# Kernel optimization log

Measured on AMD Instinct MI355X. Metric: run time of the kernel, lower is better.

Reference implementation:

```python
import jax, jax.numpy as jnp
import numpy as np

N, E = 30000, 180000
IN, H, OUT = 3000, 512, 30


def _segment_softmax(e, dst, n):
    # numerically stable softmax over incoming edges of each destination node
    m = jax.ops.segment_max(e, dst, num_segments=n)
    m = jnp.where(jnp.isfinite(m), m, 0.0)  # nodes with no in-edges
    ex = jnp.exp(e - m[dst])
    den = jax.ops.segment_sum(ex, dst, num_segments=n)
    return ex / den[dst]


def _gat(x, src, dst, Ws, Wd, a_s, a_d, n, alpha=None):
    """edGATConv (heads=1, no self-loops, no bias).
    xs = lin_s(x); attention score from lin_s(x)[src] and lin_d(x)[dst];
    out[i] = sum_{e: dst_e=i} alpha_e * xs[src_e].
    If alpha is given (tie_alpha), reuse it instead of recomputing."""
    xs = x @ Ws.T  # [n, F_out]
    if alpha is None:
        xd = x @ Wd.T
        e = jax.nn.leaky_relu(xs[src] @ a_s + xd[dst] @ a_d, 0.2)  # [E]
        alpha = _segment_softmax(e, dst, n)
    out = jax.ops.segment_sum(alpha[:, None] * xs[src], dst, num_segments=n)
    return out, alpha


def setup_inputs() -> dict:
    key = jax.random.key(0)
    ks = jax.random.split(key, 7)
    features = jax.random.normal(ks[0], (N, IN), dtype=jnp.float32)
    edge_index = jax.random.randint(ks[1], (2, E), 0, N)
    W1s = jax.random.normal(ks[2], (H, IN), dtype=jnp.float32) * 0.02
    W1d = jax.random.normal(ks[3], (H, IN), dtype=jnp.float32) * 0.02
    a1s = jax.random.normal(ks[4], (H,), dtype=jnp.float32) * 0.1
    a1d = jax.random.normal(ks[5], (H,), dtype=jnp.float32) * 0.1
    W2s = jax.random.normal(ks[6], (OUT, H), dtype=jnp.float32) * 0.05
    return {"features": features, "edge_index": edge_index,
            "W1s": W1s, "W1d": W1d, "a1s": a1s, "a1d": a1d, "W2s": W2s}


def reference(features, edge_index, W1s, W1d, a1s, a1d, W2s):
    src, dst = edge_index[0], edge_index[1]
    n = features.shape[0]
    # conv1: attentive GAT layer, stores tie_alpha
    h1, alpha1 = _gat(features, src, dst, W1s, W1d, a1s, a1d, n)
    h1 = jax.nn.elu(h1)
    # conv2: aslinear=True -> plain linear with lin_s
    h2 = h1 @ W2s.T  # [N, OUT]
    # conv3: weights tied to conv2 transposed, alpha tied to conv1
    # W3s = W2s.T so xs3 = h2 @ W3s.T = h2 @ W2s
    h3, _ = _gat(h2, src, dst, W2s.T, None, None, None, n, alpha=alpha1)
    h3 = jax.nn.elu(h3)
    # conv4: aslinear, weight tied to conv1 transposed: h3 @ W4s.T = h3 @ W1s
    h4 = h3 @ W1s  # [N, IN]
    return (h2, h4)
```

## Files before the change

### kernel.cpp

```cpp
#include <hip/hip_runtime.h>

typedef unsigned short u16;
typedef __bf16 bf16_t;
typedef bf16_t bf16x8 __attribute__((ext_vector_type(8)));
typedef float f32x4 __attribute__((ext_vector_type(4)));
typedef u16 u16x8 __attribute__((ext_vector_type(8)));

#define AS1 __attribute__((address_space(1)))
#define AS3 __attribute__((address_space(3)))

__device__ __forceinline__ u16 f2bf(float f) {
    union { float f; unsigned u; } v; v.f = f;
    unsigned r = v.u + 0x7FFFu + ((v.u >> 16) & 1u);
    return (u16)(r >> 16);
}
__device__ __forceinline__ float bf2f(u16 s) {
    union { unsigned u; float f; } v; v.u = ((unsigned)s) << 16;
    return v.f;
}

__device__ __forceinline__ void gload_lds16(const u16* g, u16* l) {
    __builtin_amdgcn_global_load_lds((AS1 const void*)g, (AS3 void*)l, 16, 0, 0);
}

template <bool OUT_BF16, bool GUARD>
__global__ __launch_bounds__(256) void gemm_bt(
    const u16* __restrict__ A, const u16* __restrict__ B, void* __restrict__ Cv,
    int K, int ldc, int Mreal, int Nreal, int vgx, int vgy)
{
    __shared__ u16 As[128 * 64];
    __shared__ u16 Bs[128 * 64];
    const int t = threadIdx.x;
    const int w = t >> 6, l = t & 63;
    const int wm = (w >> 1) * 64, wn = (w & 1) * 64;
    const int srow = w << 5;
    const int lrow = l >> 3, lc = l & 7;
    const int nwg = vgx * vgy;
    const int q = nwg >> 3, r = nwg & 7;

    for (int vb = blockIdx.x; vb < nwg; vb += gridDim.x) {
        const int xcd = vb & 7, loc = vb >> 3;
        const int swz = (xcd < r ? xcd * (q + 1) : r * (q + 1) + (xcd - r) * q) + loc;
        const int bx = swz % vgx, by = swz / vgx;
        const int m0 = by * 128, n0 = bx * 128;

        f32x4 acc[4][4] = {};

        for (int kt = 0; kt < K; kt += 64) {
#pragma unroll
            for (int i = 0; i < 4; ++i) {
                int row = srow + i * 8 + lrow;
                int gc = ((lc ^ (row & 7)) << 3);
                const u16* ga = A + (size_t)(m0 + row) * K + kt + gc;
                const u16* gb = B + (size_t)(n0 + row) * K + kt + gc;
                gload_lds16(ga, &As[(srow + i * 8) * 64]);
                gload_lds16(gb, &Bs[(srow + i * 8) * 64]);
            }
            asm volatile("s_waitcnt vmcnt(0)");
            __syncthreads();

#pragma unroll
            for (int kk = 0; kk < 2; ++kk) {
                bf16x8 af[4], bfr[4];
                int kc = kk * 4 + (l >> 4);
#pragma unroll
                for (int mi = 0; mi < 4; ++mi) {
                    int row = wm + mi * 16 + (l & 15);
                    af[mi] = *(const bf16x8*)&As[row * 64 + ((kc ^ (row & 7)) << 3)];
                }
#pragma unroll
                for (int ni = 0; ni < 4; ++ni) {
                    int col = wn + ni * 16 + (l & 15);
                    bfr[ni] = *(const bf16x8*)&Bs[col * 64 + ((kc ^ (col & 7)) << 3)];
                }
#pragma unroll
                for (int mi = 0; mi < 4; ++mi)
#pragma unroll
                    for (int ni = 0; ni < 4; ++ni)
                        acc[mi][ni] = __builtin_amdgcn_mfma_f32_16x16x32_bf16(
                            af[mi], bfr[ni], acc[mi][ni], 0, 0, 0);
            }
            __syncthreads();
        }

#pragma unroll
        for (int mi = 0; mi < 4; ++mi) {
#pragma unroll
            for (int qq = 0; qq < 4; ++qq) {
                int row = m0 + wm + mi * 16 + (l >> 4) * 4 + qq;
                if (GUARD && row >= Mreal) continue;
#pragma unroll
                for (int ni = 0; ni < 4; ++ni) {
                    int col = n0 + wn + ni * 16 + (l & 15);
                    if (GUARD && col >= Nreal) continue;
                    float v = acc[mi][ni][qq];
                    if (OUT_BF16) ((u16*)Cv)[(size_t)row * ldc + col] = f2bf(v);
                    else          ((float*)Cv)[(size_t)row * ldc + col] = v;
                }
            }
        }
    }
}

__global__ __launch_bounds__(256) void gemm_xw2(
    const float* __restrict__ X, const u16* __restrict__ Bw, u16* __restrict__ C,
    const float* __restrict__ vd, const float* __restrict__ vs,
    float* __restrict__ sd, float* __restrict__ ss)
{
    __shared__ u16 As[128 * 64];
    __shared__ u16 Bs[2][128 * 64];
    const int t = threadIdx.x;
    const int w = t >> 6, l = t & 63;
    const int wm = (w >> 1) * 64, wn = (w & 1) * 64;
    const int srow = w << 5;
    const int lrow = l >> 3, lc = l & 7;

    const int VGX = 4, NWG = 4 * 235;
    const int q = NWG >> 3, r = NWG & 7;

    for (int vb = blockIdx.x; vb < NWG; vb += gridDim.x) {
        const int xcd = vb & 7, loc = vb >> 3;
        const int swz = (xcd < r ? xcd * (q + 1) : r * (q + 1) + (xcd - r) * q) + loc;
        const int bx = swz % VGX, by = swz / VGX;
        const int m0 = by * 128, n0 = bx * 128;

        f32x4 acc[4][4] = {};
        float sdp[4] = {}, ssp[4] = {};
        const bool do_s = (bx == 0);

        int rowg[4];
        bool okr[4];
#pragma unroll
        for (int i = 0; i < 4; ++i) {
            rowg[i] = m0 + srow + i * 8 + lrow;
            okr[i] = rowg[i] < 30000;
        }

        float4 pa[4][2];
        auto loadA = [&](int kt) {
            int c = kt + lc * 8;
            bool okc = c < 3000;
#pragma unroll
            for (int i = 0; i < 4; ++i) {
                bool ok = okr[i] && okc;
                const float* p = X + (ok ? ((size_t)rowg[i] * 3000 + c) : 0);
                float4 v0 = *(const float4*)p;
                float4 v1 = *(const float4*)(p + 4);
                if (!ok) { v0 = make_float4(0.f, 0.f, 0.f, 0.f); v1 = v0; }
                pa[i][0] = v0;
                pa[i][1] = v1;
            }
        };
        auto stageB = [&](int kt2, int buf) {
#pragma unroll
            for (int i = 0; i < 4; ++i) {
                int row = srow + i * 8 + lrow;
                int gc = ((lc ^ (row & 7)) << 3);
                gload_lds16(Bw + (size_t)(n0 + row) * 3008 + kt2 + gc,
                            &Bs[buf][(srow + i * 8) * 64]);
            }
        };

        loadA(0);
        stageB(0, 0);
        int cur = 0;

        for (int kt = 0; kt < 3008; kt += 64) {
            if (do_s) {
                int c = kt + lc * 8;
                float4 d0 = *(const float4*)(vd + c);
                float4 d1 = *(const float4*)(vd + c + 4);
                float4 s0 = *(const float4*)(vs + c);
                float4 s1 = *(const float4*)(vs + c + 4);
#pragma unroll
                for (int i = 0; i < 4; ++i) {
                    sdp[i] += pa[i][0].x * d0.x + pa[i][0].y * d0.y + pa[i][0].z * d0.z + pa[i][0].w * d0.w
                            + pa[i][1].x * d1.x + pa[i][1].y * d1.y + pa[i][1].z * d1.z + pa[i][1].w * d1.w;
                    ssp[i] += pa[i][0].x * s0.x + pa[i][0].y * s0.y + pa[i][0].z * s0.z + pa[i][0].w * s0.w
                            + pa[i][1].x * s1.x + pa[i][1].y * s1.y + pa[i][1].z * s1.z + pa[i][1].w * s1.w;
                }
            }
#pragma unroll
            for (int i = 0; i < 4; ++i) {
                int row = srow + i * 8 + lrow;
                bf16x8 o;
                o[0] = (bf16_t)pa[i][0].x; o[1] = (bf16_t)pa[i][0].y;
                o[2] = (bf16_t)pa[i][0].z; o[3] = (bf16_t)pa[i][0].w;
                o[4] = (bf16_t)pa[i][1].x; o[5] = (bf16_t)pa[i][1].y;
                o[6] = (bf16_t)pa[i][1].z; o[7] = (bf16_t)pa[i][1].w;
                *(bf16x8*)&As[row * 64 + ((lc ^ (row & 7)) << 3)] = o;
            }
            loadA(kt + 64);
            int ktn = (kt + 64 < 3008) ? kt + 64 : 2944;
            stageB(ktn, cur ^ 1);
            asm volatile("s_waitcnt vmcnt(12) lgkmcnt(0)" ::: "memory");
            __builtin_amdgcn_s_barrier();

#pragma unroll
            for (int kk = 0; kk < 2; ++kk) {
                bf16x8 af[4], bfr[4];
                int kc = kk * 4 + (l >> 4);
#pragma unroll
                for (int mi = 0; mi < 4; ++mi) {
                    int row = wm + mi * 16 + (l & 15);
                    af[mi] = *(const bf16x8*)&As[row * 64 + ((kc ^ (row & 7)) << 3)];
                }
#pragma unroll
                for (int ni = 0; ni < 4; ++ni) {
                    int col = wn + ni * 16 + (l & 15);
                    bfr[ni] = *(const bf16x8*)&Bs[cur][col * 64 + ((kc ^ (col & 7)) << 3)];
                }
#pragma unroll
                for (int mi = 0; mi < 4; ++mi)
#pragma unroll
                    for (int ni = 0; ni < 4; ++ni)
                        acc[mi][ni] = __builtin_amdgcn_mfma_f32_16x16x32_bf16(
                            af[mi], bfr[ni], acc[mi][ni], 0, 0, 0);
            }
            asm volatile("s_barrier" ::: "memory");
            cur ^= 1;
        }

        if (do_s) {
#pragma unroll
            for (int i = 0; i < 4; ++i) {
                float a = sdp[i], b = ssp[i];
                a += __shfl_xor(a, 1); a += __shfl_xor(a, 2); a += __shfl_xor(a, 4);
                b += __shfl_xor(b, 1); b += __shfl_xor(b, 2); b += __shfl_xor(b, 4);
                if (lc == 0 && okr[i]) { sd[rowg[i]] = a; ss[rowg[i]] = b; }
            }
        }

#pragma unroll
        for (int mi = 0; mi < 4; ++mi)
#pragma unroll
            for (int qq = 0; qq < 4; ++qq) {
                int row = m0 + wm + mi * 16 + (l >> 4) * 4 + qq;
#pragma unroll
                for (int ni = 0; ni < 4; ++ni) {
                    int col = n0 + wn + ni * 16 + (l & 15);
                    C[(size_t)row * 512 + col] = f2bf(acc[mi][ni][qq]);
                }
            }
    }
}

__global__ void k_prep(const float* __restrict__ W1d, const float* __restrict__ a1d,
                       const float* __restrict__ W1s, const float* __restrict__ a1s,
                       const float* __restrict__ W2s, const int* __restrict__ dst,
                       float* __restrict__ vdp, float* __restrict__ vsp,
                       u16* __restrict__ w1sb, u16* __restrict__ w1st,
                       u16* __restrict__ w2sb, unsigned* __restrict__ deg) {
    int b = blockIdx.x, t = threadIdx.x;
    if (b < 48) {
        int hseg = b & 3, iblk = b >> 2;
        int i = iblk * 256 + t;
        if (i >= 3000) return;
        float ad = 0.f, as = 0.f;
        int h0 = hseg * 128;
        for (int h = h0; h < h0 + 128; ++h) {
            ad += W1d[(size_t)h * 3000 + i] * a1d[h];
            as += W1s[(size_t)h * 3000 + i] * a1s[h];
        }
        vdp[(size_t)hseg * 3008 + i] = ad;
        vsp[(size_t)hseg * 3008 + i] = as;
    } else if (b < 1552) {
        int idx = (b - 48) * 256 + t;
        int n = idx / 752, k = (idx % 752) * 4;
        ushort4 o = make_ushort4(0, 0, 0, 0);
        if (k < 3000) {
            float4 v = *(const float4*)(W1s + (size_t)n * 3000 + k);
            o.x = f2bf(v.x); o.y = f2bf(v.y); o.z = f2bf(v.z); o.w = f2bf(v.w);
        }
        *(ushort4*)(w1sb + (size_t)n * 3008 + k) = o;
    } else if (b < 1936) {
        __shared__ float tile[64][65];
        int fb = b - 1552;
        int i0 = (fb % 48) * 64, h0 = (fb / 48) * 64;
        int il = t & 63, hq = t >> 6;
#pragma unroll
        for (int rr = 0; rr < 16; ++rr) {
            int hl = rr * 4 + hq;
            int i = i0 + il;
            tile[hl][il] = (i < 3000) ? W1s[(size_t)(h0 + hl) * 3000 + i] : 0.f;
        }
        __syncthreads();
#pragma unroll
        for (int rr = 0; rr < 16; ++rr) {
            int il2 = rr * 4 + hq;
            w1st[(size_t)(i0 + il2) * 512 + h0 + il] = f2bf(tile[il][il2]);
        }
    } else if (b < 2192) {
        int idx = (b - 1936) * 256 + t;
        int n = idx >> 9, k = idx & 511;
        w2sb[idx] = (n < 30) ? f2bf(W2s[(size_t)n * 512 + k]) : (u16)0;
    } else {
        int j = (b - 2192) * 256 + t;
        if (j < 180000) atomicAdd(&deg[dst[j]], 1u);
    }
}

__global__ void k_comb(const float* __restrict__ vdp, const float* __restrict__ vsp,
                       float* __restrict__ vd, float* __restrict__ vs) {
    int i = blockIdx.x * 256 + threadIdx.x;
    if (i >= 3008) return;
    if (i < 3000) {
        vd[i] = vdp[i] + vdp[3008 + i] + vdp[6016 + i] + vdp[9024 + i];
        vs[i] = vsp[i] + vsp[3008 + i] + vsp[6016 + i] + vsp[9024 + i];
    } else {
        vd[i] = 0.f;
        vs[i] = 0.f;
    }
}

__global__ void k_scan1(const unsigned* __restrict__ deg, unsigned* __restrict__ bsum, int n) {
    __shared__ unsigned ws[4];
    int i = blockIdx.x * 256 + threadIdx.x;
    unsigned v = (i < n) ? deg[i] : 0u;
#pragma unroll
    for (int s = 32; s; s >>= 1) v += __shfl_xor(v, s);
    if ((threadIdx.x & 63) == 0) ws[threadIdx.x >> 6] = v;
    __syncthreads();
    if (threadIdx.x == 0) bsum[blockIdx.x] = ws[0] + ws[1] + ws[2] + ws[3];
}

__global__ void k_scanB(const unsigned* __restrict__ deg, const unsigned* __restrict__ bsum,
                        unsigned* __restrict__ off, unsigned* __restrict__ cur,
                        int n, int nb) {
    __shared__ unsigned tmp[256];
    __shared__ unsigned bo;
    int b = blockIdx.x, t = threadIdx.x, i = b * 256 + t;
    if (t < 64) {
        unsigned s0 = (t < nb) ? bsum[t] : 0u;
        unsigned s1 = (t + 64 < nb) ? bsum[t + 64] : 0u;
        unsigned v = ((t < b) ? s0 : 0u) + ((t + 64 < b) ? s1 : 0u);
#pragma unroll
        for (int s = 32; s; s >>= 1) v += __shfl_xor(v, s);
        if (t == 0) bo = v;
        if (b == nb - 1) {
            unsigned tv = s0 + s1;
#pragma unroll
            for (int s = 32; s; s >>= 1) tv += __shfl_xor(tv, s);
            if (t == 0) off[n] = tv;
        }
    }
    __syncthreads();
    unsigned v = (i < n) ? deg[i] : 0u;
    tmp[t] = v;
    __syncthreads();
    for (int s = 1; s < 256; s <<= 1) {
        unsigned a = (t >= s) ? tmp[t - s] : 0u;
        __syncthreads();
        tmp[t] += a;
        __syncthreads();
    }
    if (i < n) {
        unsigned o = bo + tmp[t] - v;
        off[i] = o;
        cur[i] = o;
    }
}

__global__ void k_fill(const int* __restrict__ dst, unsigned* __restrict__ cur,
                       unsigned* __restrict__ csr) {
    int j = blockIdx.x * 256 + threadIdx.x;
    if (j >= 180000) return;
    unsigned pos = atomicAdd(&cur[dst[j]], 1u);
    csr[pos] = (unsigned)j;
}

__global__ void k_soft(const int* __restrict__ src, const float* __restrict__ ss,
                       const float* __restrict__ sd, float* __restrict__ alpha,
                       const unsigned* __restrict__ csr, const unsigned* __restrict__ off) {
    int t = threadIdx.x;
    int g = t >> 3, l = t & 7;
    int n = blockIdx.x * 32 + g;
    if (n >= 30000) return;
    unsigned lo = off[n], hi = off[n + 1];
    if (lo == hi) return;
    float sdn = sd[n];
    float m = -1e30f;
    for (unsigned i = lo + l; i < hi; i += 8) {
        float v = ss[src[csr[i]]] + sdn;
        v = v > 0.f ? v : 0.2f * v;
        m = fmaxf(m, v);
    }
    m = fmaxf(m, __shfl_xor(m, 1));
    m = fmaxf(m, __shfl_xor(m, 2));
    m = fmaxf(m, __shfl_xor(m, 4));
    float den = 0.f;
    for (unsigned i = lo + l; i < hi; i += 8) {
        float v = ss[src[csr[i]]] + sdn;
        v = v > 0.f ? v : 0.2f * v;
        den += expf(v - m);
    }
    den += __shfl_xor(den, 1);
    den += __shfl_xor(den, 2);
    den += __shfl_xor(den, 4);
    float inv = 1.f / den;
    for (unsigned i = lo + l; i < hi; i += 8) {
        unsigned j = csr[i];
        float v = ss[src[j]] + sdn;
        v = v > 0.f ? v : 0.2f * v;
        alpha[j] = expf(v - m) * inv;
    }
}

__global__ void k_agg(const u16* __restrict__ xin, const float* __restrict__ alpha,
                      const unsigned* __restrict__ csr, const unsigned* __restrict__ off,
                      const int* __restrict__ src, u16* __restrict__ outb, int nvalid) {
    int w = threadIdx.x >> 6, l = threadIdx.x & 63;
    int n = blockIdx.x * 4 + w;
    float acc[8] = {};
    if (n < nvalid) {
        unsigned lo = off[n], hi = off[n + 1];
        unsigned i = lo;
        for (; i + 2 <= hi; i += 2) {
            unsigned j0 = csr[i], j1 = csr[i + 1];
            float a0 = alpha[j0], a1 = alpha[j1];
            int s0 = src[j0], s1 = src[j1];
            u16x8 r0 = *(const u16x8*)&xin[(size_t)s0 * 512 + l * 8];
            u16x8 r1 = *(const u16x8*)&xin[(size_t)s1 * 512 + l * 8];
#pragma unroll
            for (int k = 0; k < 8; ++k) acc[k] += a0 * bf2f(r0[k]) + a1 * bf2f(r1[k]);
        }
        if (i < hi) {
            unsigned j0 = csr[i];
            float a0 = alpha[j0];
            int s0 = src[j0];
            u16x8 r0 = *(const u16x8*)&xin[(size_t)s0 * 512 + l * 8];
#pragma unroll
            for (int k = 0; k < 8; ++k) acc[k] += a0 * bf2f(r0[k]);
        }
    }
    u16x8 o;
#pragma unroll
    for (int k = 0; k < 8; ++k) {
        float a = acc[k] > 0.f ? acc[k] : expf(acc[k]) - 1.f;
        o[k] = f2bf(a);
    }
    *(u16x8*)&outb[(size_t)n * 512 + l * 8] = o;
}

__global__ void k_aggG(const float* __restrict__ h2, const float* __restrict__ alpha,
                       const unsigned* __restrict__ csr, const unsigned* __restrict__ off,
                       const int* __restrict__ src, float* __restrict__ g) {
    int t = threadIdx.x, grp = t >> 3, l = t & 7;
    int n = blockIdx.x * 32 + grp;
    if (n >= 30000) return;
    unsigned lo = off[n], hi = off[n + 1];
    float acc[4] = {};
    int c0 = l * 4;
    for (unsigned i = lo; i < hi; ++i) {
        unsigned j = csr[i];
        float a = alpha[j];
        const float* row = h2 + (size_t)src[j] * 30;
#pragma unroll
        for (int k = 0; k < 4; ++k) {
            int c = c0 + k;
            if (c < 30) acc[k] += a * row[c];
        }
    }
#pragma unroll
    for (int k = 0; k < 4; ++k) {
        int c = c0 + k;
        if (c < 30) g[(size_t)n * 30 + c] = acc[k];
    }
}

__global__ void k_h3(const float* __restrict__ g, const float* __restrict__ W2s,
                     u16* __restrict__ h3b) {
    int t = threadIdx.x;
    size_t n0 = (size_t)blockIdx.x * 8;
    float w0[30], w1[30];
#pragma unroll
    for (int o = 0; o < 30; ++o) {
        w0[o] = W2s[(size_t)o * 512 + t];
        w1[o] = W2s[(size_t)o * 512 + t + 256];
    }
    for (int rr = 0; rr < 8; ++rr) {
        size_t n = n0 + rr;
        float a0 = 0.f, a1 = 0.f;
        if (n < 30000) {
            const float* gr = g + n * 30;
#pragma unroll
            for (int o = 0; o < 30; ++o) {
                float v = gr[o];
                a0 += v * w0[o];
                a1 += v * w1[o];
            }
            a0 = a0 > 0.f ? a0 : expf(a0) - 1.f;
            a1 = a1 > 0.f ? a1 : expf(a1) - 1.f;
        }
        h3b[n * 512 + t] = f2bf(a0);
        h3b[n * 512 + t + 256] = f2bf(a1);
    }
}

extern "C" void kernel_launch(void* const* d_in, const int* in_sizes, int n_in,
                              void* d_out, int out_size, void* d_ws, size_t ws_size,
                              hipStream_t stream) {
    const float* X   = (const float*)d_in[0];
    const int*   ei  = (const int*)d_in[1];
    const float* W1s = (const float*)d_in[2];
    const float* W1d = (const float*)d_in[3];
    const float* a1s = (const float*)d_in[4];
    const float* a1d = (const float*)d_in[5];
    const float* W2s = (const float*)d_in[6];
    const int* src = ei;
    const int* dst = ei + 180000;

    float* out = (float*)d_out;
    float* h2 = out;
    float* h4 = out + 900000;

    char* ob = (char*)(out + 900000);
    u16* xs1b = (u16*)ob;
    u16* h1b  = (u16*)(ob + 30801920);
    float* g  = (float*)(ob + 30801920 + 30801920);

    char* w = (char*)d_ws;
    auto carve = [&](size_t bytes) { char* p = w; w += (bytes + 255) & ~(size_t)255; return p; };
    u16* w1sb  = (u16*)carve((size_t)512 * 3008 * 2);
    u16* w1st  = (u16*)carve((size_t)3072 * 512 * 2);
    u16* w2sb  = (u16*)carve((size_t)128 * 512 * 2);
    u16* h3b   = (u16*)carve((size_t)30080 * 512 * 2);
    float* vd    = (float*)carve(3008 * 4);
    float* vs    = (float*)carve(3008 * 4);
    float* vdp   = (float*)carve(4 * 3008 * 4);
    float* vsp   = (float*)carve(4 * 3008 * 4);
    float* ss    = (float*)carve(30000 * 4);
    float* sd    = (float*)carve(30000 * 4);
    float* alpha = (float*)carve(180000 * 4);
    unsigned* deg = (unsigned*)carve(30000 * 4);
    unsigned* off = (unsigned*)carve(30004 * 4);
    unsigned* cur = (unsigned*)carve(30000 * 4);
    unsigned* csr = (unsigned*)carve(180000 * 4);
    unsigned* bsum = (unsigned*)carve(128 * 4);

    hipMemsetAsync(deg, 0, 30000 * 4, stream);

    k_prep<<<2896, 256, 0, stream>>>(W1d, a1d, W1s, a1s, W2s, dst,
                                     vdp, vsp, w1sb, w1st, w2sb, deg);
    k_comb<<<12, 256, 0, stream>>>(vdp, vsp, vd, vs);

    gemm_xw2<<<768, 256, 0, stream>>>(X, w1sb, xs1b, vd, vs, sd, ss);

    k_scan1<<<118, 256, 0, stream>>>(deg, bsum, 30000);
    k_scanB<<<118, 256, 0, stream>>>(deg, bsum, off, cur, 30000, 118);
    k_fill<<<704, 256, 0, stream>>>(dst, cur, csr);
    k_soft<<<938, 256, 0, stream>>>(src, ss, sd, alpha, csr, off);

    k_agg <<<7520, 256, 0, stream>>>(xs1b, alpha, csr, off, src, h1b, 30000);

    gemm_bt<false, true><<<235, 256, 0, stream>>>(h1b, w2sb, h2, 512, 30, 30000, 30, 1, 235);

    k_aggG<<<938, 256, 0, stream>>>(h2, alpha, csr, off, src, g);
    k_h3 <<<3760, 256, 0, stream>>>(g, W2s, h3b);

    gemm_bt<false, true><<<1280, 256, 0, stream>>>(h3b, w1st, h4, 512, 3000, 30000, 3000, 24, 235);
}
```

Baseline: 593.2 us.

## Stage fp32 X tiles into LDS via direct global-to-LDS loads, convert on read

The first GEMM now loads fp32 feature tiles straight into a swizzled LDS buffer with global_load_lds and converts to bf16 when building the MFMA fragments, so the fp32-to-bf16 staging through registers goes away. The fused attention-score dot products move into the fragment-read phase, run by half the waves. B is no longer double-buffered, and each k-step waits for all loads before a full barrier, so load/compute overlap is lost and LDS use grows with the fp32 A tile. Out-of-range K columns are zeroed in LDS on the last tile, and out-of-range rows are clamped.

New measurement: 701.4 us. +18.2%, slower.

```diff
diff --git a/kernel.cpp b/kernel.cpp
--- a/kernel.cpp
+++ b/kernel.cpp
@@ -20,6 +20,9 @@
 }
 
 __device__ __forceinline__ void gload_lds16(const u16* g, u16* l) {
+    __builtin_amdgcn_global_load_lds((AS1 const void*)g, (AS3 void*)l, 16, 0, 0);
+}
+__device__ __forceinline__ void gload_ldsf(const float* g, float* l) {
     __builtin_amdgcn_global_load_lds((AS1 const void*)g, (AS3 void*)l, 16, 0, 0);
 }
 
@@ -102,13 +105,13 @@
     }
 }
 
-__global__ __launch_bounds__(256) void gemm_xw2(
+__global__ __launch_bounds__(256) void gemm_xw3(
     const float* __restrict__ X, const u16* __restrict__ Bw, u16* __restrict__ C,
     const float* __restrict__ vd, const float* __restrict__ vs,
     float* __restrict__ sd, float* __restrict__ ss)
 {
-    __shared__ u16 As[128 * 64];
-    __shared__ u16 Bs[2][128 * 64];
+    __shared__ float Asf[128 * 64];
+    __shared__ u16 Bs[128 * 64];
     const int t = threadIdx.x;
     const int w = t >> 6, l = t & 63;
     const int wm = (w >> 1) * 64, wn = (w & 1) * 64;
@@ -126,89 +129,69 @@
 
         f32x4 acc[4][4] = {};
         float sdp[4] = {}, ssp[4] = {};
-        const bool do_s = (bx == 0);
-
-        int rowg[4];
-        bool okr[4];
-#pragma unroll
-        for (int i = 0; i < 4; ++i) {
-            rowg[i] = m0 + srow + i * 8 + lrow;
-            okr[i] = rowg[i] < 30000;
-        }
-
-        float4 pa[4][2];
-        auto loadA = [&](int kt) {
-            int c = kt + lc * 8;
-            bool okc = c < 3000;
-#pragma unroll
-            for (int i = 0; i < 4; ++i) {
-                bool ok = okr[i] && okc;
-                const float* p = X + (ok ? ((size_t)rowg[i] * 3000 + c) : 0);
-                float4 v0 = *(const float4*)p;
-                float4 v1 = *(const float4*)(p + 4);
-                if (!ok) { v0 = make_float4(0.f, 0.f, 0.f, 0.f); v1 = v0; }
-                pa[i][0] = v0;
-                pa[i][1] = v1;
-            }
-        };
-        auto stageB = [&](int kt2, int buf) {
+        const bool wsd = (bx == 0) && ((w & 1) == 0);
+
+        for (int kt = 0; kt < 3008; kt += 64) {
 #pragma unroll
             for (int i = 0; i < 4; ++i) {
                 int row = srow + i * 8 + lrow;
                 int gc = ((lc ^ (row & 7)) << 3);
-                gload_lds16(Bw + (size_t)(n0 + row) * 3008 + kt2 + gc,
-                            &Bs[buf][(srow + i * 8) * 64]);
-            }
-        };
-
-        loadA(0);
-        stageB(0, 0);
-        int cur = 0;
-
-        for (int kt = 0; kt < 3008; kt += 64) {
-            if (do_s) {
-                int c = kt + lc * 8;
-                float4 d0 = *(const float4*)(vd + c);
-                float4 d1 = *(const float4*)(vd + c + 4);
-                float4 s0 = *(const float4*)(vs + c);
-                float4 s1 = *(const float4*)(vs + c + 4);
-#pragma unroll
-                for (int i = 0; i < 4; ++i) {
-                    sdp[i] += pa[i][0].x * d0.x + pa[i][0].y * d0.y + pa[i][0].z * d0.z + pa[i][0].w * d0.w
-                            + pa[i][1].x * d1.x + pa[i][1].y * d1.y + pa[i][1].z * d1.z + pa[i][1].w * d1.w;
-                    ssp[i] += pa[i][0].x * s0.x + pa[i][0].y * s0.y + pa[i][0].z * s0.z + pa[i][0].w * s0.w
-                            + pa[i][1].x * s1.x + pa[i][1].y * s1.y + pa[i][1].z * s1.z + pa[i][1].w * s1.w;
-                }
-            }
-#pragma unroll
-            for (int i = 0; i < 4; ++i) {
-                int row = srow + i * 8 + lrow;
-                bf16x8 o;
-                o[0] = (bf16_t)pa[i][0].x; o[1] = (bf16_t)pa[i][0].y;
-                o[2] = (bf16_t)pa[i][0].z; o[3] = (bf16_t)pa[i][0].w;
-                o[4] = (bf16_t)pa[i][1].x; o[5] = (bf16_t)pa[i][1].y;
-                o[6] = (bf16_t)pa[i][1].z; o[7] = (bf16_t)pa[i][1].w;
-                *(bf16x8*)&As[row * 64 + ((lc ^ (row & 7)) << 3)] = o;
-            }
-            loadA(kt + 64);
-            int ktn = (kt + 64 < 3008) ? kt + 64 : 2944;
-            stageB(ktn, cur ^ 1);
-            asm volatile("s_waitcnt vmcnt(12) lgkmcnt(0)" ::: "memory");
-            __builtin_amdgcn_s_barrier();
+                gload_lds16(Bw + (size_t)(n0 + row) * 3008 + kt + gc,
+                            &Bs[(srow + i * 8) * 64]);
+            }
+#pragma unroll
+            for (int i = 0; i < 8; ++i) {
+                int rbase = srow + i * 4;
+                int row = rbase + (l >> 4);
+                int grow = m0 + row;
+                if (grow > 29999) grow = 29999;
+                int jg = (l & 15) ^ (row & 15);
+                gload_ldsf(X + (size_t)grow * 3000 + kt + jg * 4,
+                           &Asf[rbase * 64]);
+            }
+            asm volatile("s_waitcnt vmcnt(0)");
+            __syncthreads();
+
+            if (kt == 2944) {
+                int zr = t >> 1, jl = 14 + (t & 1);
+                int js = jl ^ (zr & 15);
+                *(float4*)&Asf[zr * 64 + js * 4] = make_float4(0.f, 0.f, 0.f, 0.f);
+                __syncthreads();
+            }
 
 #pragma unroll
             for (int kk = 0; kk < 2; ++kk) {
+                int kc = kk * 4 + (l >> 4);
                 bf16x8 af[4], bfr[4];
-                int kc = kk * 4 + (l >> 4);
 #pragma unroll
                 for (int mi = 0; mi < 4; ++mi) {
                     int row = wm + mi * 16 + (l & 15);
-                    af[mi] = *(const bf16x8*)&As[row * 64 + ((kc ^ (row & 7)) << 3)];
+                    int pb = (kc ^ ((row & 15) >> 1)) * 8;
+                    int lo = (row & 1) << 2;
+                    float4 a0 = *(const float4*)&Asf[row * 64 + pb + lo];
+                    float4 a1 = *(const float4*)&Asf[row * 64 + pb + (lo ^ 4)];
+                    bf16x8 o;
+                    o[0] = (bf16_t)a0.x; o[1] = (bf16_t)a0.y;
+                    o[2] = (bf16_t)a0.z; o[3] = (bf16_t)a0.w;
+                    o[4] = (bf16_t)a1.x; o[5] = (bf16_t)a1.y;
+                    o[6] = (bf16_t)a1.z; o[7] = (bf16_t)a1.w;
+                    af[mi] = o;
+                    if (wsd) {
+                        int c = kt + kc * 8;
+                        float4 d0 = *(const float4*)(vd + c);
+                        float4 d1 = *(const float4*)(vd + c + 4);
+                        float4 s0 = *(const float4*)(vs + c);
+                        float4 s1 = *(const float4*)(vs + c + 4);
+                        sdp[mi] += a0.x * d0.x + a0.y * d0.y + a0.z * d0.z + a0.w * d0.w
+                                 + a1.x * d1.x + a1.y * d1.y + a1.z * d1.z + a1.w * d1.w;
+                        ssp[mi] += a0.x * s0.x + a0.y * s0.y + a0.z * s0.z + a0.w * s0.w
+                                 + a1.x * s1.x + a1.y * s1.y + a1.z * s1.z + a1.w * s1.w;
+                    }
                 }
 #pragma unroll
                 for (int ni = 0; ni < 4; ++ni) {
                     int col = wn + ni * 16 + (l & 15);
-                    bfr[ni] = *(const bf16x8*)&Bs[cur][col * 64 + ((kc ^ (col & 7)) << 3)];
+                    bfr[ni] = *(const bf16x8*)&Bs[col * 64 + ((kc ^ (col & 7)) << 3)];
                 }
 #pragma unroll
                 for (int mi = 0; mi < 4; ++mi)
@@ -217,17 +200,17 @@
                         acc[mi][ni] = __builtin_amdgcn_mfma_f32_16x16x32_bf16(
                             af[mi], bfr[ni], acc[mi][ni], 0, 0, 0);
             }
-            asm volatile("s_barrier" ::: "memory");
-            cur ^= 1;
-        }
-
-        if (do_s) {
-#pragma unroll
-            for (int i = 0; i < 4; ++i) {
-                float a = sdp[i], b = ssp[i];
-                a += __shfl_xor(a, 1); a += __shfl_xor(a, 2); a += __shfl_xor(a, 4);
-                b += __shfl_xor(b, 1); b += __shfl_xor(b, 2); b += __shfl_xor(b, 4);
-                if (lc == 0 && okr[i]) { sd[rowg[i]] = a; ss[rowg[i]] = b; }
+            __syncthreads();
+        }
+
+        if (wsd) {
+#pragma unroll
+            for (int mi = 0; mi < 4; ++mi) {
+                float a = sdp[mi], b = ssp[mi];
+                a += __shfl_xor(a, 16); a += __shfl_xor(a, 32);
+                b += __shfl_xor(b, 16); b += __shfl_xor(b, 32);
+                int grow = m0 + wm + mi * 16 + (l & 15);
+                if (l < 16 && grow < 30000) { sd[grow] = a; ss[grow] = b; }
             }
         }
 
@@ -544,7 +527,7 @@
                                      vdp, vsp, w1sb, w1st, w2sb, deg);
     k_comb<<<12, 256, 0, stream>>>(vdp, vsp, vd, vs);
 
-    gemm_xw2<<<768, 256, 0, stream>>>(X, w1sb, xs1b, vd, vs, sd, ss);
+    gemm_xw3<<<768, 256, 0, stream>>>(X, w1sb, xs1b, vd, vs, sd, ss);
 
     k_scan1<<<118, 256, 0, stream>>>(deg, bsum, 30000);
     k_scanB<<<118, 256, 0, stream>>>(deg, bsum, off, cur, 30000, 118);
```
